# Kernel tuning notes

Measured on AMD Instinct MI355X. Metric: run time of the kernel, lower is better.

The kernel has to match this reference:

```python
import jax, jax.numpy as jnp
import numpy as np

LN_EPS = 1e-12


def _conv1d(x, w, b, pad):
    # x: (B, Cin, L), w: (Cout, Cin, K) -> (B, Cout, L)
    y = jax.lax.conv_general_dilated(x, w, window_strides=(1,), padding=[(pad, pad)],
                                     dimension_numbers=('NCH', 'OIH', 'NCH'))
    return y + b[None, :, None]


def setup_inputs() -> dict:
    key = jax.random.key(0)
    ks = jax.random.split(key, 6)
    B, L, C, KH = 4, 4096, 768, 7
    return {
        'hidden_states': jax.random.normal(ks[0], (B, L, C), jnp.float32),
        'attention_mask': jnp.ones((B, L), jnp.float32),
        'special_tokens_mask': jnp.zeros((B, L), jnp.float32),
        'ln_w': jnp.ones((C,), jnp.float32),
        'ln_b': jnp.zeros((C,), jnp.float32),
        'off_w': jax.random.normal(ks[1], (KH, C, KH), jnp.float32) * 0.02,
        'off_b': jnp.zeros((KH,), jnp.float32),
        'mod_w': jax.random.normal(ks[2], (KH, C, KH), jnp.float32) * 0.02,
        'mod_b': jnp.zeros((KH,), jnp.float32),
        'reg_w': jax.random.normal(ks[3], (C, C, KH), jnp.float32) * 0.02,
    }


def reference(hidden_states, attention_mask, special_tokens_mask,
              ln_w, ln_b, off_w, off_b, mod_w, mod_b, reg_w):
    B, L, C = hidden_states.shape
    kh = off_w.shape[0]
    pad = kh // 2
    residual = hidden_states

    # input layernorm (biased variance, like torch.nn.LayerNorm)
    mu = hidden_states.mean(-1, keepdims=True)
    var = hidden_states.var(-1, keepdims=True)
    h = (hidden_states - mu) * jax.lax.rsqrt(var + LN_EPS) * ln_w + ln_b

    ht = jnp.swapaxes(h, 1, 2)  # (B, C, L)
    off = _conv1d(ht, off_w, off_b, pad)                    # (B, kh, L) seq-axis offsets
    mod = 2.0 * jax.nn.sigmoid(_conv1d(ht, mod_w, mod_b, pad))  # (B, kh, L)

    # mask special tokens / padding before sampling
    gate = ((1.0 - special_tokens_mask) * attention_mask)[:, None, :]
    xm = ht * gate  # (B, C, L)

    # deformable 1D sampling positions: p - pad + k + off[b,k,p]
    base = (jnp.arange(L, dtype=jnp.float32) - pad)[None, :] + jnp.arange(kh, dtype=jnp.float32)[:, None]  # (kh, L)
    pos = base[None, :, :] + off  # (B, kh, L)
    f = jnp.floor(pos)
    t = pos - f                   # (B, kh, L) frac
    fi = f.astype(jnp.int32)

    def gather(idx):
        # linear-sample tap with zero padding outside [0, L-1]
        inb = ((idx >= 0) & (idx <= L - 1)).astype(xm.dtype)  # (B, kh, L)
        idxc = jnp.clip(idx, 0, L - 1)
        v = jax.vmap(lambda xb, ib: xb[:, ib])(xm, idxc)      # (B, C, kh, L)
        return v * inb[:, None, :, :]

    sample = gather(fi) * (1.0 - t)[:, None] + gather(fi + 1) * t[:, None]  # (B, C, kh, L)
    sample = sample * mod[:, None]  # modulated

    out = jnp.einsum('ock,bckp->bop', reg_w, sample)  # (B, C, L)
    out = jnp.swapaxes(out, 1, 2) + residual          # (B, L, C)
    return out
```

## Files before the change

kernel.cpp:

```cpp
#include <hip/hip_runtime.h>
#include <math.h>

#define BB 4
#define LL 4096
#define CC 768
#define KHH 7
#define PADK 3
#define ROWS (BB*LL)
#define NKP  (BB*KHH*LL)
#define GK   (KHH*CC)
#define NT   (GK/64)
#define NKC  (GK/8)

typedef unsigned short ushort8 __attribute__((ext_vector_type(8)));
typedef short short8 __attribute__((ext_vector_type(8)));
typedef float f32x4 __attribute__((ext_vector_type(4)));
typedef unsigned int uint4v __attribute__((ext_vector_type(4)));

__device__ __forceinline__ float bf2f(unsigned short u) {
    return __uint_as_float(((unsigned)u) << 16);
}
__device__ __forceinline__ unsigned short f2bf(float x) {
    unsigned u = __float_as_uint(x);
    return (unsigned short)((u + 0x7FFFu + ((u >> 16) & 1u)) >> 16);
}
__device__ __forceinline__ unsigned cvtpk(float lo, float hi) {
    unsigned r;
    asm("v_cvt_pk_bf16_f32 %0, %1, %2" : "=v"(r) : "v"(lo), "v"(hi));
    return r;
}

__global__ __launch_bounds__(256) void k_ln(const float* __restrict__ x,
        const float* __restrict__ mask, const float* __restrict__ special,
        const float* __restrict__ lnw, const float* __restrict__ lnb,
        unsigned short* __restrict__ hb, float* __restrict__ gate) {
    int row = blockIdx.x;
    const float* xr = x + (size_t)row * CC;
    float s = 0.f, q = 0.f;
    for (int i = threadIdx.x; i < CC; i += 256) { float v = xr[i]; s += v; q += v * v; }
    for (int o = 32; o; o >>= 1) { s += __shfl_xor(s, o); q += __shfl_xor(q, o); }
    __shared__ float ss[4], sq[4];
    int wid = threadIdx.x >> 6;
    if ((threadIdx.x & 63) == 0) { ss[wid] = s; sq[wid] = q; }
    __syncthreads();
    s = ss[0] + ss[1] + ss[2] + ss[3];
    q = sq[0] + sq[1] + sq[2] + sq[3];
    float mu  = s * (1.f / CC);
    float var = fmaxf(q * (1.f / CC) - mu * mu, 0.f);
    float rstd = rsqrtf(var + 1e-12f);
    unsigned short* hr = hb + (size_t)row * CC;
    for (int i = threadIdx.x; i < CC; i += 256)
        hr[i] = f2bf((xr[i] - mu) * rstd * lnw[i] + lnb[i]);
    if (threadIdx.x == 0) gate[row] = (1.f - special[row]) * mask[row];
}

__global__ __launch_bounds__(256) void k_wbt(const float* __restrict__ rw,
                                             unsigned short* __restrict__ wbt) {
    __shared__ float s[GK];
    int o = blockIdx.x;
    for (int i = threadIdx.x; i < GK; i += 256) s[i] = rw[(size_t)o * GK + i];
    __syncthreads();
    for (int kc = threadIdx.x; kc < NKC; kc += 256) {
        int k = kc / 96;
        int c0 = (kc - k * 96) * 8;
        ushort8 r;
#pragma unroll
        for (int e = 0; e < 8; ++e) r[e] = f2bf(s[(c0 + e) * KHH + k]);
        *(ushort8*)(wbt + ((size_t)kc * CC + o) * 8) = r;
    }
}

__global__ __launch_bounds__(256) void k_wcb(const float* __restrict__ ow, const float* __restrict__ mw,
                                             unsigned short* __restrict__ wcb) {
    int i = blockIdx.x;
    for (int c = threadIdx.x; c < CC; c += 256) {
        float v = 0.f;
        if (i < 49)      v = ow[(size_t)(i / 7) * (CC * KHH) + (size_t)c * KHH + (i % 7)];
        else if (i < 98) { int j = i - 49; v = mw[(size_t)(j / 7) * (CC * KHH) + (size_t)c * KHH + (j % 7)]; }
        wcb[(size_t)i * CC + c] = f2bf(v);
    }
}

__global__ __launch_bounds__(256) void k_dg2(const unsigned short* __restrict__ A,
        const unsigned short* __restrict__ Bm, float* __restrict__ d) {
    __shared__ __align__(16) char As[128 * 128];
    __shared__ __align__(16) char Bs[128 * 128];
    int r0 = blockIdx.x * 128;
    int t = threadIdx.x;
    int lane = t & 63, w = t >> 6;
    int wr = w >> 1, wc = w & 1;
    f32x4 acc[4][4];
#pragma unroll
    for (int m = 0; m < 4; ++m)
#pragma unroll
        for (int n = 0; n < 4; ++n) acc[m][n] = (f32x4){0.f, 0.f, 0.f, 0.f};
    int lr = lane & 15;
    int lkb0 = (lane >> 4) * 16;
    for (int kk = 0; kk < CC; kk += 64) {
#pragma unroll
        for (int s = 0; s < 4; ++s) {
            int byteoff = (s * 256 + t) * 16;
            int row = byteoff >> 7;
            int colb = byteoff & 127;
            int sw = (row * 128 + colb) ^ ((row & 7) << 4);
            *(ushort8*)(As + sw) = *(const ushort8*)(A + (size_t)(r0 + row) * CC + kk + (colb >> 1));
            *(ushort8*)(Bs + sw) = *(const ushort8*)(Bm + (size_t)row * CC + kk + (colb >> 1));
        }
        __syncthreads();
#pragma unroll
        for (int ks = 0; ks < 2; ++ks) {
            short8 av[4], bv[4];
            int lkb = lkb0 + ks * 64;
#pragma unroll
            for (int m = 0; m < 4; ++m) {
                int ar = wr * 64 + m * 16 + lr;
                av[m] = *(const short8*)(As + ((ar * 128 + lkb) ^ ((ar & 7) << 4)));
            }
#pragma unroll
            for (int n = 0; n < 4; ++n) {
                int br = wc * 64 + n * 16 + lr;
                bv[n] = *(const short8*)(Bs + ((br * 128 + lkb) ^ ((br & 7) << 4)));
            }
#pragma unroll
            for (int m = 0; m < 4; ++m)
#pragma unroll
                for (int n = 0; n < 4; ++n)
                    acc[m][n] = __builtin_amdgcn_mfma_f32_16x16x32_bf16(av[m], bv[n], acc[m][n], 0, 0, 0);
        }
        __syncthreads();
    }
    int lr4 = (lane >> 4) * 4, lc = lane & 15;
#pragma unroll
    for (int m = 0; m < 4; ++m) {
        int gr = r0 + wr * 64 + m * 16 + lr4;
#pragma unroll
        for (int n = 0; n < 4; ++n) {
            int gc = wc * 64 + n * 16 + lc;
#pragma unroll
            for (int j = 0; j < 4; ++j)
                d[(size_t)(gr + j) * 128 + gc] = acc[m][n][j];
        }
    }
}

__global__ __launch_bounds__(256) void k_off(const float* __restrict__ d,
        const float* __restrict__ offb, const float* __restrict__ modb,
        const float* __restrict__ gate,
        int* __restrict__ idx0, int* __restrict__ idx1,
        float* __restrict__ w0a, float* __restrict__ w1a) {
    int flat = blockIdx.x * 256 + threadIdx.x;
    if (flat >= NKP) return;
    int p = flat & (LL - 1);
    int k = (flat >> 12) % KHH;
    int b = flat / (KHH * LL);
    float offa = offb[k], moda = modb[k];
#pragma unroll
    for (int j = 0; j < KHH; ++j) {
        int q = p + j - PADK;
        if (q >= 0 && q < LL) {
            const float* dr = d + (size_t)(b * LL + q) * 128;
            offa += dr[k * 7 + j];
            moda += dr[49 + k * 7 + j];
        }
    }
    float modv = 2.f / (1.f + expf(-moda));
    float pos = (float)(p - PADK + k) + offa;
    pos = fminf(fmaxf(pos, -1.0e9f), 1.0e9f);
    float f = floorf(pos);
    float tf = pos - f;
    int i0 = (int)f;
    int i1 = i0 + 1;
    float in0 = (i0 >= 0 && i0 < LL) ? 1.f : 0.f;
    float in1 = (i1 >= 0 && i1 < LL) ? 1.f : 0.f;
    int c0 = min(max(i0, 0), LL - 1);
    int c1 = min(max(i1, 0), LL - 1);
    float g0 = gate[b * LL + c0] * in0;
    float g1 = gate[b * LL + c1] * in1;
    w0a[flat] = modv * (1.f - tf) * g0;
    w1a[flat] = modv * tf * g1;
    idx0[flat] = c0;
    idx1[flat] = c1;
}


#define STEPOFF 49152
#define KSOFF   24576

#define LOADB3(Q, KS, D0, D1, D2) do { \
    const unsigned short* _q = (Q) + (KS) * KSOFF; \
    D0 = *(const short8*)(_q); \
    D1 = *(const short8*)(_q + 128); \
    D2 = *(const short8*)(_q + 256); \
} while (0)

#define MFMA_ROW3(AV, M, B0, B1, B2) \
    acc[M][0] = __builtin_amdgcn_mfma_f32_16x16x32_bf16(AV, B0, acc[M][0], 0, 0, 0); \
    acc[M][1] = __builtin_amdgcn_mfma_f32_16x16x32_bf16(AV, B1, acc[M][1], 0, 0, 0); \
    acc[M][2] = __builtin_amdgcn_mfma_f32_16x16x32_bf16(AV, B2, acc[M][2], 0, 0, 0);

#define COMPUTE_KS3(ASB, KS, B0, B1, B2) do { \
    __builtin_amdgcn_s_setprio(1); \
    int _lkb = ke0 * 2 + (KS) * 64; \
    short8 _av0, _av1, _av2, _av3, _av4, _av5, _av6, _av7; \
    { int ar = 0 * 16 + lr; _av0 = *(const short8*)((ASB) + ar * 128 + (_lkb ^ ((ar & 7) << 4))); } \
    { int ar = 1 * 16 + lr; _av1 = *(const short8*)((ASB) + ar * 128 + (_lkb ^ ((ar & 7) << 4))); } \
    { int ar = 2 * 16 + lr; _av2 = *(const short8*)((ASB) + ar * 128 + (_lkb ^ ((ar & 7) << 4))); } \
    { int ar = 3 * 16 + lr; _av3 = *(const short8*)((ASB) + ar * 128 + (_lkb ^ ((ar & 7) << 4))); } \
    MFMA_ROW3(_av0, 0, B0, B1, B2) \
    MFMA_ROW3(_av1, 1, B0, B1, B2) \
    MFMA_ROW3(_av2, 2, B0, B1, B2) \
    MFMA_ROW3(_av3, 3, B0, B1, B2) \
    { int ar = 4 * 16 + lr; _av4 = *(const short8*)((ASB) + ar * 128 + (_lkb ^ ((ar & 7) << 4))); } \
    { int ar = 5 * 16 + lr; _av5 = *(const short8*)((ASB) + ar * 128 + (_lkb ^ ((ar & 7) << 4))); } \
    { int ar = 6 * 16 + lr; _av6 = *(const short8*)((ASB) + ar * 128 + (_lkb ^ ((ar & 7) << 4))); } \
    { int ar = 7 * 16 + lr; _av7 = *(const short8*)((ASB) + ar * 128 + (_lkb ^ ((ar & 7) << 4))); } \
    MFMA_ROW3(_av4, 4, B0, B1, B2) \
    MFMA_ROW3(_av5, 5, B0, B1, B2) \
    MFMA_ROW3(_av6, 6, B0, B1, B2) \
    MFMA_ROW3(_av7, 7, B0, B1, B2) \
    __builtin_amdgcn_s_setprio(0); \
} while (0)

#define BAR() do { \
    asm volatile("s_waitcnt lgkmcnt(0)" ::: "memory"); \
    __builtin_amdgcn_s_barrier(); \
    __builtin_amdgcn_sched_barrier(0); \
} while (0)

__global__ __launch_bounds__(512, 2) void k_fgemm(const unsigned short* __restrict__ hb,
        const unsigned short* __restrict__ Wbt,
        const int* __restrict__ idx0, const int* __restrict__ idx1,
        const float* __restrict__ w0a, const float* __restrict__ w1a,
        const float* __restrict__ resid, float* __restrict__ out) {
    __shared__ __align__(16) char As[2][128 * 128];

    int bid = blockIdx.x;
    int nhalf = (bid & 7) >> 2;
    int rowtile = (bid >> 3) * 4 + (bid & 3);
    int r0 = rowtile * 128;
    int o0 = nhalf * 384;
    int b = r0 >> 12;
    int p0 = r0 & (LL - 1);
    int pbase = ((b * KHH) << 12) + p0;
    const unsigned short* hbB = hb + (size_t)b * LL * CC;

    int t = threadIdx.x;
    int lane = t & 63, wc = t >> 6;
    int lr = lane & 15;
    int ke0 = (lane >> 4) * 8;

    const unsigned short* pB = Wbt + ((size_t)(lane >> 4) * CC + o0 + wc * 48 + lr) * 8;

    int arow = t >> 2, aseg = t & 3;
    int acolb = aseg * 32;
    int aswz0 = arow * 128 + (acolb ^ ((arow & 7) << 4));
    int aswz1 = arow * 128 + ((acolb + 16) ^ ((arow & 7) << 4));

    f32x4 acc[8][3];
#pragma unroll
    for (int m = 0; m < 8; ++m)
#pragma unroll
        for (int n = 0; n < 3; ++n) acc[m][n] = (f32x4){0.f, 0.f, 0.f, 0.f};

    float wa = 0.f, wbv = 0.f;
    int cur_tap = -1;
    const unsigned short* pA0 = hbB;
    const unsigned short* pA1 = hbB;

    ushort8 la0, la1, la2, la3;
    short8 S0_0, S0_1, S0_2;
    short8 S1_0, S1_1, S1_2;
    short8 S2_0, S2_1, S2_2;

    auto loadA = [&](int tap, int c0) {
        if (tap != cur_tap) {
            int pf = pbase + (tap << 12) + arow;
            int g0 = idx0[pf], g1 = idx1[pf];
            wa = w0a[pf];  wbv = w1a[pf];
            cur_tap = tap;
            pA0 = hbB + (size_t)g0 * CC + c0 + aseg * 16;
            pA1 = hbB + (size_t)g1 * CC + c0 + aseg * 16;
        } else {
            pA0 += 64;
            pA1 += 64;
        }
        la0 = *(const ushort8*)(pA0);
        la1 = *(const ushort8*)(pA0 + 8);
        la2 = *(const ushort8*)(pA1);
        la3 = *(const ushort8*)(pA1 + 8);
    };

    auto writeA = [&](char* Asb) {
        uint4v va, vb;
#pragma unroll
        for (int p = 0; p < 4; ++p) {
            float lo = fmaf(wa, bf2f(la0[2 * p]),     wbv * bf2f(la2[2 * p]));
            float hi = fmaf(wa, bf2f(la0[2 * p + 1]), wbv * bf2f(la2[2 * p + 1]));
            va[p] = cvtpk(lo, hi);
        }
#pragma unroll
        for (int p = 0; p < 4; ++p) {
            float lo = fmaf(wa, bf2f(la1[2 * p]),     wbv * bf2f(la3[2 * p]));
            float hi = fmaf(wa, bf2f(la1[2 * p + 1]), wbv * bf2f(la3[2 * p + 1]));
            vb[p] = cvtpk(lo, hi);
        }
        *(uint4v*)(Asb + aswz0) = va;
        *(uint4v*)(Asb + aswz1) = vb;
    };

    loadA(0, 0);
    LOADB3(pB, 0, S0_0, S0_1, S0_2);
    LOADB3(pB, 1, S1_0, S1_1, S1_2);
    writeA(As[0]);
    BAR();

    int tap_c = 0, c0_c = 0;
    for (int sp = 0; sp < NT; sp += 2) {
        {
            int tap_n = tap_c, c0_n = c0_c + 64;
            if (c0_n == CC) { c0_n = 0; ++tap_n; }
            bool more = (sp + 1 < NT);
            const unsigned short* pN = pB + STEPOFF;
            if (more) {
                LOADB3(pN, 0, S2_0, S2_1, S2_2);
                loadA(tap_n, c0_n);
            }
            __builtin_amdgcn_sched_barrier(0);
            COMPUTE_KS3(As[0], 0, S0_0, S0_1, S0_2);
            COMPUTE_KS3(As[0], 1, S1_0, S1_1, S1_2);
            if (more) {
                LOADB3(pN, 1, S1_0, S1_1, S1_2);
                writeA(As[1]);
            }
            BAR();
            pB = pN;
            tap_c = tap_n; c0_c = c0_n;
        }
        {
            int s = sp + 1;
            if (s >= NT) break;
            int tap_n = tap_c, c0_n = c0_c + 64;
            if (c0_n == CC) { c0_n = 0; ++tap_n; }
            bool more = (s + 1 < NT);
            const unsigned short* pN = pB + STEPOFF;
            if (more) {
                LOADB3(pN, 0, S0_0, S0_1, S0_2);
                loadA(tap_n, c0_n);
            }
            __builtin_amdgcn_sched_barrier(0);
            COMPUTE_KS3(As[1], 0, S2_0, S2_1, S2_2);
            COMPUTE_KS3(As[1], 1, S1_0, S1_1, S1_2);
            if (more) {
                LOADB3(pN, 1, S1_0, S1_1, S1_2);
                writeA(As[0]);
            }
            BAR();
            pB = pN;
            tap_c = tap_n; c0_c = c0_n;
        }
    }

    int lr4 = (lane >> 4) * 4, lc = lane & 15;
#pragma unroll
    for (int m = 0; m < 8; ++m) {
        int gr = r0 + m * 16 + lr4;
#pragma unroll
        for (int n = 0; n < 3; ++n) {
            int gc = o0 + wc * 48 + n * 16 + lc;
#pragma unroll
            for (int j = 0; j < 4; ++j) {
                size_t idx = (size_t)(gr + j) * CC + gc;
                out[idx] = acc[m][n][j] + resid[idx];
            }
        }
    }
}

extern "C" void kernel_launch(void* const* d_in, const int* in_sizes, int n_in,
                              void* d_out, int out_size, void* d_ws, size_t ws_size,
                              hipStream_t stream) {
    const float* x   = (const float*)d_in[0];
    const float* am  = (const float*)d_in[1];
    const float* stm = (const float*)d_in[2];
    const float* lnw = (const float*)d_in[3];
    const float* lnb = (const float*)d_in[4];
    const float* ow  = (const float*)d_in[5];
    const float* ob  = (const float*)d_in[6];
    const float* mw  = (const float*)d_in[7];
    const float* mb  = (const float*)d_in[8];
    const float* rw  = (const float*)d_in[9];
    float* out = (float*)d_out;

    char* ws = (char*)d_ws;
    size_t off = 0;
    auto carve = [&](size_t bytes) -> char* {
        char* p = ws + off;
        off += (bytes + 255) & ~(size_t)255;
        return p;
    };
    unsigned short* hb  = (unsigned short*)carve((size_t)ROWS * CC * 2);
    unsigned short* wbt = (unsigned short*)carve((size_t)NKC * CC * 8 * 2);
    unsigned short* wcb = (unsigned short*)carve((size_t)128 * CC * 2);
    float* d    = (float*)carve((size_t)ROWS * 128 * 4);
    float* gate = (float*)carve((size_t)ROWS * 4);
    int*   i0   = (int*)carve((size_t)NKP * 4);
    int*   i1   = (int*)carve((size_t)NKP * 4);
    float* w0   = (float*)carve((size_t)NKP * 4);
    float* w1   = (float*)carve((size_t)NKP * 4);

    k_ln<<<ROWS, 256, 0, stream>>>(x, am, stm, lnw, lnb, hb, gate);
    k_wbt<<<CC, 256, 0, stream>>>(rw, wbt);
    k_wcb<<<128, 256, 0, stream>>>(ow, mw, wcb);
    k_dg2<<<ROWS / 128, 256, 0, stream>>>(hb, wcb, d);
    k_off<<<NKP / 256, 256, 0, stream>>>(d, ob, mb, gate, i0, i1, w0, w1);
    k_fgemm<<<256, 512, 0, stream>>>(hb, wbt, i0, i1, w0, w1, x, out);
}
```

Before: 196.7 us.

## Streamline preprocessing kernels: wave-sized layernorm, batched weight transpose, smaller GEMM tiles

Layernorm now runs one 64-thread wave per row, loading the row as three float4 registers, reducing with shuffles only (no shared memory or barrier), and storing bf16 four at a time. The weight transpose kernel handles four output channels per block so each 16-byte store covers adjacent channels and fewer blocks are launched. The small offset/modulation GEMM uses 64-row tiles instead of 128, doubling the block count to fill more CUs. These target the auxiliary kernels, not the main gather GEMM, and raise shared memory per block in the transpose kernel (about 86 KB).

```diff
diff --git a/kernel.cpp b/kernel.cpp
--- a/kernel.cpp
+++ b/kernel.cpp
@@ -13,6 +13,7 @@
 #define NKC  (GK/8)
 
 typedef unsigned short ushort8 __attribute__((ext_vector_type(8)));
+typedef unsigned short ushort4v __attribute__((ext_vector_type(4)));
 typedef short short8 __attribute__((ext_vector_type(8)));
 typedef float f32x4 __attribute__((ext_vector_type(4)));
 typedef unsigned int uint4v __attribute__((ext_vector_type(4)));
@@ -30,43 +31,60 @@
     return r;
 }
 
-__global__ __launch_bounds__(256) void k_ln(const float* __restrict__ x,
+__global__ __launch_bounds__(64) void k_ln(const float* __restrict__ x,
         const float* __restrict__ mask, const float* __restrict__ special,
         const float* __restrict__ lnw, const float* __restrict__ lnb,
         unsigned short* __restrict__ hb, float* __restrict__ gate) {
     int row = blockIdx.x;
-    const float* xr = x + (size_t)row * CC;
-    float s = 0.f, q = 0.f;
-    for (int i = threadIdx.x; i < CC; i += 256) { float v = xr[i]; s += v; q += v * v; }
+    int t = threadIdx.x;
+    const float4* xr = (const float4*)(x + (size_t)row * CC);
+    float4 v0 = xr[t], v1 = xr[t + 64], v2 = xr[t + 128];
+    float s = v0.x + v0.y + v0.z + v0.w
+            + v1.x + v1.y + v1.z + v1.w
+            + v2.x + v2.y + v2.z + v2.w;
+    float q = v0.x * v0.x + v0.y * v0.y + v0.z * v0.z + v0.w * v0.w
+            + v1.x * v1.x + v1.y * v1.y + v1.z * v1.z + v1.w * v1.w
+            + v2.x * v2.x + v2.y * v2.y + v2.z * v2.z + v2.w * v2.w;
     for (int o = 32; o; o >>= 1) { s += __shfl_xor(s, o); q += __shfl_xor(q, o); }
-    __shared__ float ss[4], sq[4];
-    int wid = threadIdx.x >> 6;
-    if ((threadIdx.x & 63) == 0) { ss[wid] = s; sq[wid] = q; }
-    __syncthreads();
-    s = ss[0] + ss[1] + ss[2] + ss[3];
-    q = sq[0] + sq[1] + sq[2] + sq[3];
     float mu  = s * (1.f / CC);
     float var = fmaxf(q * (1.f / CC) - mu * mu, 0.f);
     float rstd = rsqrtf(var + 1e-12f);
-    unsigned short* hr = hb + (size_t)row * CC;
-    for (int i = threadIdx.x; i < CC; i += 256)
-        hr[i] = f2bf((xr[i] - mu) * rstd * lnw[i] + lnb[i]);
-    if (threadIdx.x == 0) gate[row] = (1.f - special[row]) * mask[row];
+    const float4* lw = (const float4*)lnw;
+    const float4* lb = (const float4*)lnb;
+    ushort4v* hr = (ushort4v*)(hb + (size_t)row * CC);
+#pragma unroll
+    for (int j = 0; j < 3; ++j) {
+        int i4 = t + 64 * j;
+        float4 v = (j == 0) ? v0 : (j == 1) ? v1 : v2;
+        float4 w = lw[i4], bso = lb[i4];
+        ushort4v r;
+        r[0] = f2bf((v.x - mu) * rstd * w.x + bso.x);
+        r[1] = f2bf((v.y - mu) * rstd * w.y + bso.y);
+        r[2] = f2bf((v.z - mu) * rstd * w.z + bso.z);
+        r[3] = f2bf((v.w - mu) * rstd * w.w + bso.w);
+        hr[i4] = r;
+    }
+    if (t == 0) gate[row] = (1.f - special[row]) * mask[row];
 }
 
 __global__ __launch_bounds__(256) void k_wbt(const float* __restrict__ rw,
                                              unsigned short* __restrict__ wbt) {
-    __shared__ float s[GK];
-    int o = blockIdx.x;
-    for (int i = threadIdx.x; i < GK; i += 256) s[i] = rw[(size_t)o * GK + i];
+    __shared__ float s[4 * GK];
+    int o0 = blockIdx.x * 4;
+    for (int i = threadIdx.x; i < 4 * GK; i += 256)
+        s[i] = rw[(size_t)(o0 + i / GK) * GK + (i % GK)];
     __syncthreads();
     for (int kc = threadIdx.x; kc < NKC; kc += 256) {
         int k = kc / 96;
         int c0 = (kc - k * 96) * 8;
-        ushort8 r;
-#pragma unroll
-        for (int e = 0; e < 8; ++e) r[e] = f2bf(s[(c0 + e) * KHH + k]);
-        *(ushort8*)(wbt + ((size_t)kc * CC + o) * 8) = r;
+        unsigned short* dst = wbt + ((size_t)kc * CC + o0) * 8;
+#pragma unroll
+        for (int oo = 0; oo < 4; ++oo) {
+            ushort8 r;
+#pragma unroll
+            for (int e = 0; e < 8; ++e) r[e] = f2bf(s[oo * GK + (c0 + e) * KHH + k]);
+            *(ushort8*)(dst + oo * 8) = r;
+        }
     }
 }
 
@@ -83,37 +101,44 @@
 
 __global__ __launch_bounds__(256) void k_dg2(const unsigned short* __restrict__ A,
         const unsigned short* __restrict__ Bm, float* __restrict__ d) {
-    __shared__ __align__(16) char As[128 * 128];
+    __shared__ __align__(16) char As[64 * 128];
     __shared__ __align__(16) char Bs[128 * 128];
-    int r0 = blockIdx.x * 128;
+    int r0 = blockIdx.x * 64;
     int t = threadIdx.x;
     int lane = t & 63, w = t >> 6;
     int wr = w >> 1, wc = w & 1;
-    f32x4 acc[4][4];
-#pragma unroll
-    for (int m = 0; m < 4; ++m)
+    f32x4 acc[2][4];
+#pragma unroll
+    for (int m = 0; m < 2; ++m)
 #pragma unroll
         for (int n = 0; n < 4; ++n) acc[m][n] = (f32x4){0.f, 0.f, 0.f, 0.f};
     int lr = lane & 15;
     int lkb0 = (lane >> 4) * 16;
     for (int kk = 0; kk < CC; kk += 64) {
+#pragma unroll
+        for (int s = 0; s < 2; ++s) {
+            int byteoff = (s * 256 + t) * 16;
+            int row = byteoff >> 7;
+            int colb = byteoff & 127;
+            int sw = (row * 128 + colb) ^ ((row & 7) << 4);
+            *(ushort8*)(As + sw) = *(const ushort8*)(A + (size_t)(r0 + row) * CC + kk + (colb >> 1));
+        }
 #pragma unroll
         for (int s = 0; s < 4; ++s) {
             int byteoff = (s * 256 + t) * 16;
             int row = byteoff >> 7;
             int colb = byteoff & 127;
             int sw = (row * 128 + colb) ^ ((row & 7) << 4);
-            *(ushort8*)(As + sw) = *(const ushort8*)(A + (size_t)(r0 + row) * CC + kk + (colb >> 1));
             *(ushort8*)(Bs + sw) = *(const ushort8*)(Bm + (size_t)row * CC + kk + (colb >> 1));
         }
         __syncthreads();
 #pragma unroll
         for (int ks = 0; ks < 2; ++ks) {
-            short8 av[4], bv[4];
+            short8 av[2], bv[4];
             int lkb = lkb0 + ks * 64;
 #pragma unroll
-            for (int m = 0; m < 4; ++m) {
-                int ar = wr * 64 + m * 16 + lr;
+            for (int m = 0; m < 2; ++m) {
+                int ar = wr * 32 + m * 16 + lr;
                 av[m] = *(const short8*)(As + ((ar * 128 + lkb) ^ ((ar & 7) << 4)));
             }
 #pragma unroll
@@ -122,7 +147,7 @@
                 bv[n] = *(const short8*)(Bs + ((br * 128 + lkb) ^ ((br & 7) << 4)));
             }
 #pragma unroll
-            for (int m = 0; m < 4; ++m)
+            for (int m = 0; m < 2; ++m)
 #pragma unroll
                 for (int n = 0; n < 4; ++n)
                     acc[m][n] = __builtin_amdgcn_mfma_f32_16x16x32_bf16(av[m], bv[n], acc[m][n], 0, 0, 0);
@@ -131,8 +156,8 @@
     }
     int lr4 = (lane >> 4) * 4, lc = lane & 15;
 #pragma unroll
-    for (int m = 0; m < 4; ++m) {
-        int gr = r0 + wr * 64 + m * 16 + lr4;
+    for (int m = 0; m < 2; ++m) {
+        int gr = r0 + wr * 32 + m * 16 + lr4;
 #pragma unroll
         for (int n = 0; n < 4; ++n) {
             int gc = wc * 64 + n * 16 + lc;
@@ -408,10 +433,10 @@
     float* w0   = (float*)carve((size_t)NKP * 4);
     float* w1   = (float*)carve((size_t)NKP * 4);
 
-    k_ln<<<ROWS, 256, 0, stream>>>(x, am, stm, lnw, lnb, hb, gate);
-    k_wbt<<<CC, 256, 0, stream>>>(rw, wbt);
+    k_ln<<<ROWS, 64, 0, stream>>>(x, am, stm, lnw, lnb, hb, gate);
+    k_wbt<<<CC / 4, 256, 0, stream>>>(rw, wbt);
     k_wcb<<<128, 256, 0, stream>>>(ow, mw, wcb);
-    k_dg2<<<ROWS / 128, 256, 0, stream>>>(hb, wcb, d);
+    k_dg2<<<ROWS / 64, 256, 0, stream>>>(hb, wcb, d);
     k_off<<<NKP / 256, 256, 0, stream>>>(d, ob, mb, gate, i0, i1, w0, w1);
     k_fgemm<<<256, 512, 0, stream>>>(hb, wbt, i0, i1, w0, w1, x, out);
 }
```

After: 184.9 us. 6.0% less time.
